# Kernel tuning notes

Hardware: AMD Instinct MI355X
Metric: run time of the kernel (lower is better)

Reference implementation:

```python
import jax, jax.numpy as jnp
import numpy as np

B, C, N, K = 4, 64, 8192, 16
OUT = 128

def setup_inputs() -> dict:
    key = jax.random.key(0)
    k1, k2, k3, k4 = jax.random.split(key, 4)
    x = jax.random.normal(k1, (B, C, N, 1), dtype=jnp.float32)
    edge_index = jax.random.randint(k2, (2, B, N, K), 0, N)
    # BasicConv([2C, OUT]) is a 1x1 Conv2d -> weight [OUT, 2C], bias [OUT]
    W_nn = jax.random.normal(k3, (OUT, 2 * C), dtype=jnp.float32) * 0.02
    b_nn = jax.random.normal(k4, (OUT,), dtype=jnp.float32) * 0.02
    return {"x": x, "edge_index": edge_index, "W_nn": W_nn, "b_nn": b_nn}

def _gather_nodes(x2, idx):
    # x2: [B, C, N], idx: [B, N, K] -> [B, C, N, K]
    return jax.vmap(lambda xb, ib: xb[:, ib])(x2, idx)

def reference(x, edge_index, W_nn, b_nn):
    b, c, n, _ = x.shape
    x2 = x[:, :, :, 0]                      # [B, C, N]
    x_i = _gather_nodes(x2, edge_index[1])  # [B, C, N, K]
    x_j = _gather_nodes(x2, edge_index[0])  # [B, C, N, K]
    x_j = jnp.max(x_j - x_i, axis=-1, keepdims=True)  # [B, C, N, 1]
    # interleave channels: cat([x.unsqueeze(2), x_j.unsqueeze(2)], dim=2).reshape(b, 2c, n, 1)
    h = jnp.concatenate([x[:, :, None], x_j[:, :, None]], axis=2).reshape(b, 2 * c, n, 1)
    # BasicConv: 1x1 conv + bias + ReLU
    out = jnp.einsum('oc,bcn->bon', W_nn, h[:, :, :, 0]) + b_nn[None, :, None]
    return jax.nn.relu(out)[:, :, :, None]  # [B, OUT, N, 1]
```

## Files before the change

kernel.cpp:

```cpp
#include <hip/hip_runtime.h>
#include <cstddef>

#define BB 4
#define CC 64
#define NN 8192
#define KK 16
#define OO 128

#define SH 136

typedef __attribute__((ext_vector_type(8))) short bf16x8;
typedef __attribute__((ext_vector_type(4))) float f32x4;

__device__ __forceinline__ unsigned short f2b(float f) {
    unsigned u = __builtin_bit_cast(unsigned, f);
    unsigned r = (u + 0x7fffu + ((u >> 16) & 1u)) >> 16;
    return (unsigned short)r;
}

__device__ __forceinline__ float bclo(unsigned d) {
    return __builtin_bit_cast(float, d << 16);
}
__device__ __forceinline__ float bchi(unsigned d) {
    return __builtin_bit_cast(float, d & 0xffff0000u);
}

__global__ __launch_bounds__(256) void transpose_kernel(
        const float* __restrict__ x, unsigned short* __restrict__ xt,
        const float* __restrict__ W, unsigned short* __restrict__ Wbf) {
    __shared__ float tile[64][65];
    const int b  = blockIdx.y;
    const int n0 = blockIdx.x * 64;
    const int t  = threadIdx.x;
    const int ln = t & 63;
    const int r  = t >> 6;

    const float* xb = x + (size_t)b * CC * NN;
    #pragma unroll
    for (int s = 0; s < 64; s += 4) {
        int c = s + r;
        tile[c][ln] = xb[(size_t)c * NN + n0 + ln];
    }
    __syncthreads();
    unsigned short* xtb = xt + ((size_t)b * NN + n0) * CC;
    #pragma unroll
    for (int s = 0; s < 64; s += 4) {
        int n = s + r;
        xtb[n * CC + ln] = f2b(tile[ln][n]);
    }

    if (b == 0 && blockIdx.x < 16) {
        int idx = blockIdx.x * 1024 + t * 4;
        float4 v = *reinterpret_cast<const float4*>(W + idx);
        ushort4 o;
        o.x = f2b(v.x); o.y = f2b(v.y); o.z = f2b(v.z); o.w = f2b(v.w);
        *reinterpret_cast<ushort4*>(Wbf + idx) = o;
    }
}

__global__ __launch_bounds__(512, 4) void main_kernel(
        const unsigned short* __restrict__ xt,
        const unsigned short* __restrict__ Wbf,
        const int*            __restrict__ eidx,
        const float*          __restrict__ bias,
        float*                __restrict__ out) {
    __shared__ unsigned short hl[64 * SH];
    __shared__ int eL[2048];

    const int t    = threadIdx.x;
    const int lane = t & 63;
    const int w    = t >> 6;
    const int b    = blockIdx.y;
    const int n_base = blockIdx.x * 64;

    const int quad = lane >> 4;
    const int l15  = lane & 15;
    const int o0   = w * 16;

    bf16x8 afr[4];
    #pragma unroll
    for (int ks = 0; ks < 4; ks++)
        afr[ks] = *reinterpret_cast<const bf16x8*>(
            Wbf + (o0 + l15) * 128 + ks * 32 + quad * 8);
    f32x4 bv = *reinterpret_cast<const f32x4*>(bias + o0 + quad * 4);

    const int* e0 = eidx + ((size_t)b * NN + n_base) * KK;
    const int* e1 = e0 + (size_t)BB * NN * KK;
    if (t < 256) {
        *reinterpret_cast<int4*>(&eL[t * 4]) =
            *reinterpret_cast<const int4*>(e0 + t * 4);
    } else {
        int u = t - 256;
        *reinterpret_cast<int4*>(&eL[1024 + u * 4]) =
            *reinterpret_cast<const int4*>(e1 + u * 4);
    }

    const unsigned short* xtb = xt + (size_t)b * NN * CC;
    const int nl = t >> 3;
    const int p  = t & 7;
    uint4 xr = *reinterpret_cast<const uint4*>(xtb + (size_t)(n_base + nl) * CC + p * 8);

    __syncthreads();

    float m[8];
    #pragma unroll
    for (int j = 0; j < 8; j++) m[j] = -1e30f;

    #pragma unroll
    for (int k = 0; k < KK; k++) {
        int ij = eL[nl * KK + k];
        int ii = eL[1024 + nl * KK + k];
        uint4 xj = *reinterpret_cast<const uint4*>(xtb + (size_t)ij * CC + p * 8);
        uint4 xi = *reinterpret_cast<const uint4*>(xtb + (size_t)ii * CC + p * 8);
        m[0] = fmaxf(m[0], bclo(xj.x) - bclo(xi.x));
        m[1] = fmaxf(m[1], bchi(xj.x) - bchi(xi.x));
        m[2] = fmaxf(m[2], bclo(xj.y) - bclo(xi.y));
        m[3] = fmaxf(m[3], bchi(xj.y) - bchi(xi.y));
        m[4] = fmaxf(m[4], bclo(xj.z) - bclo(xi.z));
        m[5] = fmaxf(m[5], bchi(xj.z) - bchi(xi.z));
        m[6] = fmaxf(m[6], bclo(xj.w) - bclo(xi.w));
        m[7] = fmaxf(m[7], bchi(xj.w) - bchi(xi.w));
    }

    unsigned xs[8];
    xs[0] = xr.x & 0xffffu; xs[1] = xr.x >> 16;
    xs[2] = xr.y & 0xffffu; xs[3] = xr.y >> 16;
    xs[4] = xr.z & 0xffffu; xs[5] = xr.z >> 16;
    xs[6] = xr.w & 0xffffu; xs[7] = xr.w >> 16;
    unsigned od[8];
    #pragma unroll
    for (int j = 0; j < 8; j++)
        od[j] = xs[j] | ((unsigned)f2b(m[j]) << 16);

    {
        unsigned short* dst = &hl[nl * SH + p * 16];
        uint4 lo, hi;
        lo.x = od[0]; lo.y = od[1]; lo.z = od[2]; lo.w = od[3];
        hi.x = od[4]; hi.y = od[5]; hi.z = od[6]; hi.w = od[7];
        *reinterpret_cast<uint4*>(dst)     = lo;
        *reinterpret_cast<uint4*>(dst + 8) = hi;
    }
    __syncthreads();

    #pragma unroll
    for (int nt = 0; nt < 4; nt++) {
        f32x4 acc = {0.f, 0.f, 0.f, 0.f};
        #pragma unroll
        for (int ks = 0; ks < 4; ks++) {
            const unsigned short* bp = &hl[(nt * 16 + l15) * SH + ks * 32 + quad * 8];
            bf16x8 bfr = *reinterpret_cast<const bf16x8*>(bp);
            acc = __builtin_amdgcn_mfma_f32_16x16x32_bf16(afr[ks], bfr, acc, 0, 0, 0);
        }
        int n_g = n_base + nt * 16 + l15;
        #pragma unroll
        for (int r = 0; r < 4; r++) {
            int o = o0 + quad * 4 + r;
            float v = acc[r] + bv[r];
            out[((size_t)b * OO + o) * NN + n_g] = fmaxf(v, 0.f);
        }
    }
}

extern "C" void kernel_launch(void* const* d_in, const int* in_sizes, int n_in,
                              void* d_out, int out_size, void* d_ws, size_t ws_size,
                              hipStream_t stream) {
    const float* x    = (const float*)d_in[0];
    const int*   eidx = (const int*)d_in[1];
    const float* W    = (const float*)d_in[2];
    const float* bias = (const float*)d_in[3];
    float* out = (float*)d_out;

    unsigned short* xt  = (unsigned short*)d_ws;
    unsigned short* Wbf = (unsigned short*)((char*)d_ws + 4 * 1024 * 1024);

    transpose_kernel<<<dim3(NN / 64, BB), dim3(256), 0, stream>>>(x, xt, W, Wbf);
    main_kernel<<<dim3(NN / 64, BB), dim3(512), 0, stream>>>(xt, Wbf, eidx, bias, out);
}
```

Measured before the change: 85.40 us.

## Double-buffer neighbor gathers, vectorize transpose stores, use nontemporal loads/stores

```diff
diff --git a/kernel.cpp b/kernel.cpp
--- a/kernel.cpp
+++ b/kernel.cpp
@@ -11,6 +11,7 @@
 
 typedef __attribute__((ext_vector_type(8))) short bf16x8;
 typedef __attribute__((ext_vector_type(4))) float f32x4;
+typedef __attribute__((ext_vector_type(4))) int   i32x4;
 
 __device__ __forceinline__ unsigned short f2b(float f) {
     unsigned u = __builtin_bit_cast(unsigned, f);
@@ -43,10 +44,17 @@
     }
     __syncthreads();
     unsigned short* xtb = xt + ((size_t)b * NN + n0) * CC;
-    #pragma unroll
-    for (int s = 0; s < 64; s += 4) {
-        int n = s + r;
-        xtb[n * CC + ln] = f2b(tile[ln][n]);
+    const int c4 = (t & 15) * 4;
+    const int nn = t >> 4;
+    #pragma unroll
+    for (int s = 0; s < 64; s += 16) {
+        int n = s + nn;
+        ushort4 o;
+        o.x = f2b(tile[c4 + 0][n]);
+        o.y = f2b(tile[c4 + 1][n]);
+        o.z = f2b(tile[c4 + 2][n]);
+        o.w = f2b(tile[c4 + 3][n]);
+        *reinterpret_cast<ushort4*>(xtb + n * CC + c4) = o;
     }
 
     if (b == 0 && blockIdx.x < 16) {
@@ -55,6 +63,30 @@
         ushort4 o;
         o.x = f2b(v.x); o.y = f2b(v.y); o.z = f2b(v.z); o.w = f2b(v.w);
         *reinterpret_cast<ushort4*>(Wbf + idx) = o;
+    }
+}
+
+template<int KB>
+__device__ __forceinline__ void loadb(uint4* XJ, uint4* XI, const unsigned short* xtb,
+                                      const int* ejp, const int* eip, int p) {
+    #pragma unroll
+    for (int q = 0; q < 4; q++) {
+        XJ[q] = *reinterpret_cast<const uint4*>(xtb + (size_t)ejp[KB + q] * CC + p * 8);
+        XI[q] = *reinterpret_cast<const uint4*>(xtb + (size_t)eip[KB + q] * CC + p * 8);
+    }
+}
+
+__device__ __forceinline__ void consume(const uint4* XJ, const uint4* XI, float* m) {
+    #pragma unroll
+    for (int q = 0; q < 4; q++) {
+        m[0] = fmaxf(m[0], bclo(XJ[q].x) - bclo(XI[q].x));
+        m[1] = fmaxf(m[1], bchi(XJ[q].x) - bchi(XI[q].x));
+        m[2] = fmaxf(m[2], bclo(XJ[q].y) - bclo(XI[q].y));
+        m[3] = fmaxf(m[3], bchi(XJ[q].y) - bchi(XI[q].y));
+        m[4] = fmaxf(m[4], bclo(XJ[q].z) - bclo(XI[q].z));
+        m[5] = fmaxf(m[5], bchi(XJ[q].z) - bchi(XI[q].z));
+        m[6] = fmaxf(m[6], bclo(XJ[q].w) - bclo(XI[q].w));
+        m[7] = fmaxf(m[7], bchi(XJ[q].w) - bchi(XI[q].w));
     }
 }
 
@@ -77,50 +109,49 @@
     const int l15  = lane & 15;
     const int o0   = w * 16;
 
+    const int* e0 = eidx + ((size_t)b * NN + n_base) * KK;
+    const int* e1 = e0 + (size_t)BB * NN * KK;
+    if (t < 256) {
+        i32x4 v = __builtin_nontemporal_load(
+            reinterpret_cast<const i32x4*>(e0 + t * 4));
+        *reinterpret_cast<i32x4*>(&eL[t * 4]) = v;
+    } else {
+        int u = t - 256;
+        i32x4 v = __builtin_nontemporal_load(
+            reinterpret_cast<const i32x4*>(e1 + u * 4));
+        *reinterpret_cast<i32x4*>(&eL[1024 + u * 4]) = v;
+    }
+
+    const unsigned short* xtb = xt + (size_t)b * NN * CC;
+    const int nl = t >> 3;
+    const int p  = t & 7;
+    uint4 xr = *reinterpret_cast<const uint4*>(xtb + (size_t)(n_base + nl) * CC + p * 8);
+
+    __syncthreads();
+
+    const int* ejp = &eL[nl * KK];
+    const int* eip = &eL[1024 + nl * KK];
+
+    float m[8];
+    #pragma unroll
+    for (int j = 0; j < 8; j++) m[j] = -1e30f;
+
+    uint4 xjA[4], xiA[4], xjB[4], xiB[4];
+    loadb<0>(xjA, xiA, xtb, ejp, eip, p);
+    loadb<4>(xjB, xiB, xtb, ejp, eip, p);
+    consume(xjA, xiA, m);
+    loadb<8>(xjA, xiA, xtb, ejp, eip, p);
+    consume(xjB, xiB, m);
+    loadb<12>(xjB, xiB, xtb, ejp, eip, p);
+    consume(xjA, xiA, m);
+    consume(xjB, xiB, m);
+
     bf16x8 afr[4];
     #pragma unroll
     for (int ks = 0; ks < 4; ks++)
         afr[ks] = *reinterpret_cast<const bf16x8*>(
             Wbf + (o0 + l15) * 128 + ks * 32 + quad * 8);
     f32x4 bv = *reinterpret_cast<const f32x4*>(bias + o0 + quad * 4);
-
-    const int* e0 = eidx + ((size_t)b * NN + n_base) * KK;
-    const int* e1 = e0 + (size_t)BB * NN * KK;
-    if (t < 256) {
-        *reinterpret_cast<int4*>(&eL[t * 4]) =
-            *reinterpret_cast<const int4*>(e0 + t * 4);
-    } else {
-        int u = t - 256;
-        *reinterpret_cast<int4*>(&eL[1024 + u * 4]) =
-            *reinterpret_cast<const int4*>(e1 + u * 4);
-    }
-
-    const unsigned short* xtb = xt + (size_t)b * NN * CC;
-    const int nl = t >> 3;
-    const int p  = t & 7;
-    uint4 xr = *reinterpret_cast<const uint4*>(xtb + (size_t)(n_base + nl) * CC + p * 8);
-
-    __syncthreads();
-
-    float m[8];
-    #pragma unroll
-    for (int j = 0; j < 8; j++) m[j] = -1e30f;
-
-    #pragma unroll
-    for (int k = 0; k < KK; k++) {
-        int ij = eL[nl * KK + k];
-        int ii = eL[1024 + nl * KK + k];
-        uint4 xj = *reinterpret_cast<const uint4*>(xtb + (size_t)ij * CC + p * 8);
-        uint4 xi = *reinterpret_cast<const uint4*>(xtb + (size_t)ii * CC + p * 8);
-        m[0] = fmaxf(m[0], bclo(xj.x) - bclo(xi.x));
-        m[1] = fmaxf(m[1], bchi(xj.x) - bchi(xi.x));
-        m[2] = fmaxf(m[2], bclo(xj.y) - bclo(xi.y));
-        m[3] = fmaxf(m[3], bchi(xj.y) - bchi(xi.y));
-        m[4] = fmaxf(m[4], bclo(xj.z) - bclo(xi.z));
-        m[5] = fmaxf(m[5], bchi(xj.z) - bchi(xi.z));
-        m[6] = fmaxf(m[6], bclo(xj.w) - bclo(xi.w));
-        m[7] = fmaxf(m[7], bchi(xj.w) - bchi(xi.w));
-    }
 
     unsigned xs[8];
     xs[0] = xr.x & 0xffffu; xs[1] = xr.x >> 16;
@@ -155,8 +186,8 @@
         #pragma unroll
         for (int r = 0; r < 4; r++) {
             int o = o0 + quad * 4 + r;
-            float v = acc[r] + bv[r];
-            out[((size_t)b * OO + o) * NN + n_g] = fmaxf(v, 0.f);
+            float v = fmaxf(acc[r] + bv[r], 0.f);
+            __builtin_nontemporal_store(v, &out[((size_t)b * OO + o) * NN + n_g]);
         }
     }
 }
```

Result: faster. 80.97 us (median of 2 runs) (-5.2%).
